# Performance work log

Hardware: AMD Instinct MI355X
Metric: run time of the kernel (lower is better)

The kernel has to match this reference:

```python
import jax, jax.numpy as jnp
import numpy as np

N_NODES = 20000
NUM_DRUGS = 2048
NUM_DPI = 200000
IN_C = 256
EMB = 256
HID = 512
OUT = 1
N_CL = 8
B = 16384


def setup_inputs() -> dict:
    key = jax.random.key(0)
    ks = jax.random.split(key, 10)
    x = jax.random.normal(ks[0], (N_NODES, IN_C), jnp.float32)
    # bipartite DPI edges: drug ids in [0, NUM_DRUGS), protein ids in [NUM_DRUGS, N_NODES)
    d = jax.random.randint(ks[1], (NUM_DPI,), 0, NUM_DRUGS)
    p = jax.random.randint(ks[2], (NUM_DPI,), NUM_DRUGS, N_NODES)
    edge_index = jnp.concatenate([jnp.stack([d, p]), jnp.stack([p, d])], axis=1)  # [2, 2*NUM_DPI]
    drug_drug_batch = jax.random.randint(ks[3], (2, B), 0, NUM_DRUGS)
    edge_cell_lines = jax.random.randint(ks[4], (B,), 0, N_CL)
    Wg1 = jax.random.normal(ks[5], (IN_C, EMB), jnp.float32) / np.float32(np.sqrt(IN_C))
    bg1 = jnp.zeros((EMB,), jnp.float32)
    Wg2 = jax.random.normal(ks[6], (EMB, EMB), jnp.float32) / np.float32(np.sqrt(EMB))
    bg2 = jnp.zeros((EMB,), jnp.float32)
    W1 = jax.random.normal(ks[7], (N_CL, 2 * EMB, HID), jnp.float32) / np.float32(np.sqrt(2 * EMB))
    b1 = jnp.zeros((N_CL, HID), jnp.float32)
    W2 = jax.random.normal(ks[8], (N_CL, HID, OUT), jnp.float32) / np.float32(np.sqrt(HID))
    b2 = jnp.zeros((N_CL, OUT), jnp.float32)
    return dict(x=x, edge_index=edge_index, drug_drug_batch=drug_drug_batch,
                edge_cell_lines=edge_cell_lines, num_drugs=NUM_DRUGS,
                Wg1=Wg1, bg1=bg1, Wg2=Wg2, bg2=bg2, W1=W1, b1=b1, W2=W2, b2=b2)


def _gcn(h_in, row, col, W, b, n):
    # PyG GCNConv: self-loops already appended to (row, col); symmetric normalization.
    h = h_in @ W  # [N, EMB]
    deg = jax.ops.segment_sum(jnp.ones(col.shape[0], h.dtype), col, num_segments=n)
    dinv = jnp.where(deg > 0, jax.lax.rsqrt(jnp.maximum(deg, 1e-12)), 0.0)
    msg = h[row] * (dinv[row] * dinv[col])[:, None]
    return jax.ops.segment_sum(msg, col, num_segments=n) + b


def reference(x, edge_index, drug_drug_batch, edge_cell_lines, num_drugs,
              Wg1, bg1, Wg2, bg2, W1, b1, W2, b2):
    n = x.shape[0]
    ar = jnp.arange(n, dtype=edge_index.dtype)
    row = jnp.concatenate([edge_index[0], ar])
    col = jnp.concatenate([edge_index[1], ar])
    h = jax.nn.relu(_gcn(x, row, col, Wg1, bg1, n))
    h = jax.nn.relu(_gcn(h, row, col, Wg2, bg2, n))
    # scatter-mean pool node embeddings of proteins into per-drug graph embeddings
    num_dpi = edge_index.shape[1] // 2
    avg = jnp.sort(edge_index[:, :num_dpi], axis=0)  # row0=drug id, row1=protein id
    node_emb = h[avg[1]]  # [NUM_DPI, EMB]
    sums = jax.ops.segment_sum(node_emb, avg[0], num_segments=num_drugs)
    cnt = jax.ops.segment_sum(jnp.ones(num_dpi, h.dtype), avg[0], num_segments=num_drugs)
    graph = sums / jnp.maximum(cnt, 1.0)[:, None]  # [NUM_DRUGS, EMB]
    xcat = jnp.concatenate([graph[drug_drug_batch[0]], graph[drug_drug_batch[1]]], axis=1)  # [B, 2*EMB]
    # per-cell-line MLP routing: run each expert over all rows, then gather per-row expert output
    n_cl = W1.shape[0]
    outs = jnp.stack([jax.nn.relu(xcat @ W1[c] + b1[c]) @ W2[c] + b2[c] for c in range(n_cl)])  # [C, B, OUT]
    preds = outs[edge_cell_lines, jnp.arange(xcat.shape[0])]  # [B, OUT]
    return preds
```

## Files before the change

### kernel.cpp

```cpp
#include <hip/hip_runtime.h>
#include <hip/hip_bf16.h>

#define N_NODES 20000
#define NUM_DRUGS 2048
#define N_PROT (N_NODES - NUM_DRUGS)
#define NUM_DPI 200000
#define E2 400000
#define CDIM 256
#define HID 512
#define N_CL 8
#define BATCH 16384
#define HN 8192

#define STRD 32
#define STRP 16
#define ELLD 192
#define ELLP 48

#define NB_T64 512
#define NB_TWG 32
#define NB_ZERO 79
#define NB_SPLIT 20000

typedef __attribute__((ext_vector_type(8))) short short8;
typedef __attribute__((ext_vector_type(4))) float floatx4;

__device__ inline unsigned short f2bf(float f) {
    unsigned u = __float_as_uint(f);
    u += 0x7fff + ((u >> 16) & 1);
    return (unsigned short)(u >> 16);
}
__device__ inline float bf2f(unsigned short h) {
    return __uint_as_float((unsigned)h << 16);
}
__device__ inline void split2(float v, unsigned short& h, unsigned short& l) {
    h = f2bf(v);
    l = f2bf(v - bf2f(h));
}
__device__ inline void gload16(const void* g, void* l) {
    __builtin_amdgcn_global_load_lds(
        (const __attribute__((address_space(1))) void*)g,
        (__attribute__((address_space(3))) void*)l, 16, 0, 0);
}
__device__ inline float4 f4fma(float4 v, float s, float4 a) {
    a.x = fmaf(v.x, s, a.x); a.y = fmaf(v.y, s, a.y);
    a.z = fmaf(v.z, s, a.z); a.w = fmaf(v.w, s, a.w);
    return a;
}
__device__ inline float4 bf4(const unsigned short* p) {
    ushort4 q = *(const ushort4*)p;
    return make_float4(bf2f(q.x), bf2f(q.y), bf2f(q.z), bf2f(q.w));
}

__global__ __launch_bounds__(256) void prep_all(
        const float* __restrict__ x, unsigned short* __restrict__ xhi,
        unsigned short* __restrict__ xlo,
        const float* __restrict__ Wg1, const float* __restrict__ Wg2,
        unsigned short* __restrict__ wg1Th, unsigned short* __restrict__ wg1Tl,
        unsigned short* __restrict__ wg2Th, unsigned short* __restrict__ wg2Tl,
        const float* __restrict__ W1, unsigned short* __restrict__ W1Th,
        unsigned short* __restrict__ W1Tl,
        int* __restrict__ cur_d, int* __restrict__ cur_p) {
    __shared__ float ld[64 * 65];
    int b = blockIdx.x;
    int t = threadIdx.x;
    int tx = t & 63, ty = t >> 6;
    if (b < NB_T64) {
        int m = b >> 5;
        int k0 = (b & 3) * 64, n0 = ((b >> 2) & 7) * 64;
        const float* Wm = W1 + (size_t)m * CDIM * HID;
#pragma unroll
        for (int rr = 0; rr < 16; rr++) {
            int kl = rr * 4 + ty;
            ld[tx * 65 + kl] = Wm[(size_t)(k0 + kl) * HID + n0 + tx];
        }
        __syncthreads();
        size_t obase = (size_t)m * HID * CDIM;
#pragma unroll
        for (int rr = 0; rr < 16; rr++) {
            int nl = rr * 4 + ty;
            float v = ld[nl * 65 + tx];
            unsigned short h, l;
            split2(v, h, l);
            size_t o = obase + (size_t)(n0 + nl) * CDIM + k0 + tx;
            W1Th[o] = h;
            W1Tl[o] = l;
        }
        return;
    }
    b -= NB_T64;
    if (b < NB_TWG) {
        const float* W = (b >> 4) ? Wg2 : Wg1;
        unsigned short* hi = (b >> 4) ? wg2Th : wg1Th;
        unsigned short* lo = (b >> 4) ? wg2Tl : wg1Tl;
        int k0 = (b & 3) * 64, n0 = ((b >> 2) & 3) * 64;
#pragma unroll
        for (int rr = 0; rr < 16; rr++) {
            int kl = rr * 4 + ty;
            ld[tx * 65 + kl] = W[(size_t)(k0 + kl) * CDIM + n0 + tx];
        }
        __syncthreads();
#pragma unroll
        for (int rr = 0; rr < 16; rr++) {
            int nl = rr * 4 + ty;
            float v = ld[nl * 65 + tx];
            unsigned short h, l;
            split2(v, h, l);
            size_t o = (size_t)(n0 + nl) * CDIM + k0 + tx;
            hi[o] = h;
            lo[o] = l;
        }
        return;
    }
    b -= NB_TWG;
    if (b < NB_ZERO) {
        int i = b * 256 + t;
        if (i < N_NODES) cur_p[i * STRP] = 0;
        if (i < NUM_DRUGS) cur_d[i * STRD] = 0;
        return;
    }
    b -= NB_ZERO;
    {
        int i = b * 256 + t;
        unsigned short h, l;
        split2(x[i], h, l);
        xhi[i] = h;
        xlo[i] = l;
    }
}

__global__ void fill_ell(const int* __restrict__ ei, int* cur_d, int* adj_drug,
                         int* cur_p, int* adj_prot) {
    int e = blockIdx.x * blockDim.x + threadIdx.x;
    if (e >= NUM_DPI) return;
    int d = ei[e];
    int p = ei[E2 + e];
    int posd = atomicAdd(&cur_d[d * STRD], 1);
    int posp = atomicAdd(&cur_p[p * STRP], 1);
    if (posd < ELLD) adj_drug[d * ELLD + posd] = p;
    if (posp < ELLP) adj_prot[(size_t)p * ELLP + posp] = d;
}

__global__ __launch_bounds__(256) void gemm_mfma(
        const unsigned short* __restrict__ Ahi, const unsigned short* __restrict__ Alo,
        const unsigned short* __restrict__ BThi, const unsigned short* __restrict__ BTlo,
        float* __restrict__ C, unsigned short* __restrict__ Cbf,
        int M, int K, int N, int mTiles,
        const int* __restrict__ cur_d, const int* __restrict__ cur_p,
        float* __restrict__ dinv) {
    if ((int)blockIdx.x >= mTiles) {
        int i = (((int)blockIdx.x - mTiles) * (int)gridDim.y + (int)blockIdx.y) * 256
                + (int)threadIdx.x;
        if (i < N_NODES) {
            int deg = (i < NUM_DRUGS) ? cur_d[i * STRD] : cur_p[i * STRP];
            dinv[i] = rsqrtf((float)(deg + 1));
        }
        return;
    }
    __shared__ unsigned short sAh[4096], sAl[4096], sBh[4096], sBl[4096];
    int t = threadIdx.x;
    int wv = t >> 6, lane = t & 63, quad = lane >> 4, l15 = lane & 15;
    int m0 = blockIdx.x * 128, n0 = blockIdx.y * 128;
    int m0w = (wv >> 1) * 64, n0w = (wv & 1) * 64;
    floatx4 zero = {0.f, 0.f, 0.f, 0.f};
    floatx4 acc[4][4];
#pragma unroll
    for (int i = 0; i < 4; i++)
#pragma unroll
        for (int j = 0; j < 4; j++) acc[i][j] = zero;

    for (int kk = 0; kk < K; kk += 32) {
#pragma unroll
        for (int c = 0; c < 2; c++) {
            int s = t + c * 256;
            int row = s >> 2, pos = s & 3;
            int ch = pos ^ ((row >> 1) & 3);
            int arow = m0 + row; if (arow > M - 1) arow = M - 1;
            int brow = n0 + row; if (brow > N - 1) brow = N - 1;
            size_t aoff = (size_t)arow * K + kk + ch * 8;
            size_t boff = (size_t)brow * K + kk + ch * 8;
            gload16(Ahi + aoff, &sAh[s * 8]);
            gload16(Alo + aoff, &sAl[s * 8]);
            gload16(BThi + boff, &sBh[s * 8]);
            gload16(BTlo + boff, &sBl[s * 8]);
        }
        __syncthreads();
        short8 ah[4], al[4], bh[4], bl[4];
        int posq = quad ^ ((l15 >> 1) & 3);
#pragma unroll
        for (int i = 0; i < 4; i++) {
            int sl = (m0w + i * 16 + l15) * 4 + posq;
            ah[i] = *(const short8*)&sAh[sl * 8];
            al[i] = *(const short8*)&sAl[sl * 8];
        }
#pragma unroll
        for (int j = 0; j < 4; j++) {
            int sl = (n0w + j * 16 + l15) * 4 + posq;
            bh[j] = *(const short8*)&sBh[sl * 8];
            bl[j] = *(const short8*)&sBl[sl * 8];
        }
#pragma unroll
        for (int i = 0; i < 4; i++)
#pragma unroll
            for (int j = 0; j < 4; j++) {
                acc[i][j] = __builtin_amdgcn_mfma_f32_16x16x32_bf16(ah[i], bh[j], acc[i][j], 0, 0, 0);
                acc[i][j] = __builtin_amdgcn_mfma_f32_16x16x32_bf16(ah[i], bl[j], acc[i][j], 0, 0, 0);
                acc[i][j] = __builtin_amdgcn_mfma_f32_16x16x32_bf16(al[i], bh[j], acc[i][j], 0, 0, 0);
            }
        __syncthreads();
    }
#pragma unroll
    for (int i = 0; i < 4; i++) {
        int gr = m0 + m0w + i * 16 + quad * 4;
#pragma unroll
        for (int r = 0; r < 4; r++) {
            if (gr + r < M) {
#pragma unroll
                for (int j = 0; j < 4; j++) {
                    size_t o = (size_t)(gr + r) * N + n0 + n0w + j * 16 + l15;
                    float v = acc[i][j][r];
                    if (C) C[o] = v;
                    if (Cbf) Cbf[o] = f2bf(v);
                }
            }
        }
    }
}

__global__ __launch_bounds__(256) void aggregate1(const float* __restrict__ tmp,
                                                  const unsigned short* __restrict__ tmpbf,
                                                  const int* __restrict__ cur_d,
                                                  const int* __restrict__ adj_drug,
                                                  const int* __restrict__ cur_p,
                                                  const int* __restrict__ adj_prot,
                                                  const float* __restrict__ dinv,
                                                  const float* __restrict__ bias,
                                                  unsigned short* __restrict__ outhi,
                                                  unsigned short* __restrict__ outlo) {
    int i = (blockIdx.x * blockDim.x + threadIdx.x) >> 6;
    int lane = threadIdx.x & 63;
    if (i >= N_NODES) return;
    float di = dinv[i];
    float4 a0 = make_float4(0.f, 0.f, 0.f, 0.f);
    float4 a1 = a0, a2 = a0, a3 = a0;
    if (i < NUM_DRUGS) {
        const int* adj = adj_drug + (size_t)i * ELLD;
        int e = cur_d[i * STRD];
        int idx = 0;
        for (; idx + 4 <= e; idx += 4) {
            int j0 = adj[idx + 0], j1 = adj[idx + 1];
            int j2 = adj[idx + 2], j3 = adj[idx + 3];
            float d0 = dinv[j0], d1 = dinv[j1], d2 = dinv[j2], d3 = dinv[j3];
            float4 v0 = bf4(&tmpbf[(size_t)j0 * CDIM + lane * 4]);
            float4 v1 = bf4(&tmpbf[(size_t)j1 * CDIM + lane * 4]);
            float4 v2 = bf4(&tmpbf[(size_t)j2 * CDIM + lane * 4]);
            float4 v3 = bf4(&tmpbf[(size_t)j3 * CDIM + lane * 4]);
            a0 = f4fma(v0, d0, a0);
            a1 = f4fma(v1, d1, a1);
            a2 = f4fma(v2, d2, a2);
            a3 = f4fma(v3, d3, a3);
        }
        for (; idx < e; idx++) {
            int j = adj[idx];
            a0 = f4fma(bf4(&tmpbf[(size_t)j * CDIM + lane * 4]), dinv[j], a0);
        }
    } else {
        const int* adj = adj_prot + (size_t)i * ELLP;
        int e = cur_p[i * STRP];
        int idx = 0;
        for (; idx + 4 <= e; idx += 4) {
            int j0 = adj[idx + 0], j1 = adj[idx + 1];
            int j2 = adj[idx + 2], j3 = adj[idx + 3];
            float d0 = dinv[j0], d1 = dinv[j1], d2 = dinv[j2], d3 = dinv[j3];
            float4 v0 = ((const float4*)(tmp + (size_t)j0 * CDIM))[lane];
            float4 v1 = ((const float4*)(tmp + (size_t)j1 * CDIM))[lane];
            float4 v2 = ((const float4*)(tmp + (size_t)j2 * CDIM))[lane];
            float4 v3 = ((const float4*)(tmp + (size_t)j3 * CDIM))[lane];
            a0 = f4fma(v0, d0, a0);
            a1 = f4fma(v1, d1, a1);
            a2 = f4fma(v2, d2, a2);
            a3 = f4fma(v3, d3, a3);
        }
        for (; idx < e; idx++) {
            int j = adj[idx];
            a0 = f4fma(((const float4*)(tmp + (size_t)j * CDIM))[lane], dinv[j], a0);
        }
    }
    float4 self = ((const float4*)(tmp + (size_t)i * CDIM))[lane];
    float4 acc;
    acc.x = (a0.x + a1.x) + (a2.x + a3.x) + self.x * di;
    acc.y = (a0.y + a1.y) + (a2.y + a3.y) + self.y * di;
    acc.z = (a0.z + a1.z) + (a2.z + a3.z) + self.z * di;
    acc.w = (a0.w + a1.w) + (a2.w + a3.w) + self.w * di;
    float4 bv = ((const float4*)bias)[lane];
    float4 r;
    r.x = fmaxf(fmaf(acc.x, di, bv.x), 0.f);
    r.y = fmaxf(fmaf(acc.y, di, bv.y), 0.f);
    r.z = fmaxf(fmaf(acc.z, di, bv.z), 0.f);
    r.w = fmaxf(fmaf(acc.w, di, bv.w), 0.f);
    ushort4 h, l;
    split2(r.x, h.x, l.x); split2(r.y, h.y, l.y);
    split2(r.z, h.z, l.z); split2(r.w, h.w, l.w);
    *(ushort4*)&outhi[(size_t)i * CDIM + lane * 4] = h;
    *(ushort4*)&outlo[(size_t)i * CDIM + lane * 4] = l;
}

__global__ __launch_bounds__(256) void aggregate2p(const float* __restrict__ tmp2,
                                                   const int* __restrict__ cur_p,
                                                   const int* __restrict__ adj_prot,
                                                   const float* __restrict__ dinv,
                                                   const float* __restrict__ bias,
                                                   unsigned short* __restrict__ h2bf) {
    int w = (blockIdx.x * blockDim.x + threadIdx.x) >> 6;
    int lane = threadIdx.x & 63;
    if (w >= N_PROT) return;
    int i = NUM_DRUGS + w;
    float di = dinv[i];
    float4 a0 = make_float4(0.f, 0.f, 0.f, 0.f);
    float4 a1 = a0, a2 = a0, a3 = a0;
    const int* adj = adj_prot + (size_t)i * ELLP;
    int e = cur_p[i * STRP];
    int idx = 0;
    for (; idx + 4 <= e; idx += 4) {
        int j0 = adj[idx + 0], j1 = adj[idx + 1];
        int j2 = adj[idx + 2], j3 = adj[idx + 3];
        float d0 = dinv[j0], d1 = dinv[j1], d2 = dinv[j2], d3 = dinv[j3];
        float4 v0 = ((const float4*)(tmp2 + (size_t)j0 * CDIM))[lane];
        float4 v1 = ((const float4*)(tmp2 + (size_t)j1 * CDIM))[lane];
        float4 v2 = ((const float4*)(tmp2 + (size_t)j2 * CDIM))[lane];
        float4 v3 = ((const float4*)(tmp2 + (size_t)j3 * CDIM))[lane];
        a0 = f4fma(v0, d0, a0);
        a1 = f4fma(v1, d1, a1);
        a2 = f4fma(v2, d2, a2);
        a3 = f4fma(v3, d3, a3);
    }
    for (; idx < e; idx++) {
        int j = adj[idx];
        a0 = f4fma(((const float4*)(tmp2 + (size_t)j * CDIM))[lane], dinv[j], a0);
    }
    float4 self = ((const float4*)(tmp2 + (size_t)i * CDIM))[lane];
    float4 acc;
    acc.x = (a0.x + a1.x) + (a2.x + a3.x) + self.x * di;
    acc.y = (a0.y + a1.y) + (a2.y + a3.y) + self.y * di;
    acc.z = (a0.z + a1.z) + (a2.z + a3.z) + self.z * di;
    acc.w = (a0.w + a1.w) + (a2.w + a3.w) + self.w * di;
    float4 bv = ((const float4*)bias)[lane];
    ushort4 o;
    o.x = f2bf(fmaxf(fmaf(acc.x, di, bv.x), 0.f));
    o.y = f2bf(fmaxf(fmaf(acc.y, di, bv.y), 0.f));
    o.z = f2bf(fmaxf(fmaf(acc.z, di, bv.z), 0.f));
    o.w = f2bf(fmaxf(fmaf(acc.w, di, bv.w), 0.f));
    *(ushort4*)&h2bf[(size_t)i * CDIM + lane * 4] = o;
}

__global__ __launch_bounds__(256) void pool_drugs(const unsigned short* __restrict__ h2bf,
                                                  unsigned short* __restrict__ Ghi,
                                                  unsigned short* __restrict__ Glo,
                                                  const int* __restrict__ cur_d,
                                                  const int* __restrict__ adj_drug) {
    __shared__ float4 red[4][64];
    int d = blockIdx.x;
    int w = threadIdx.x >> 6, lane = threadIdx.x & 63;
    const int* adj = adj_drug + (size_t)d * ELLD;
    int ecnt = cur_d[d * STRD];
    int e = ecnt < ELLD ? ecnt : ELLD;
    float4 a0 = make_float4(0.f, 0.f, 0.f, 0.f);
    float4 a1 = a0, a2 = a0, a3 = a0;
    int idx = w;
    for (; idx + 12 < e; idx += 16) {
        int j0 = adj[idx], j1 = adj[idx + 4], j2 = adj[idx + 8], j3 = adj[idx + 12];
        float4 v0 = bf4(&h2bf[(size_t)j0 * CDIM + lane * 4]);
        float4 v1 = bf4(&h2bf[(size_t)j1 * CDIM + lane * 4]);
        float4 v2 = bf4(&h2bf[(size_t)j2 * CDIM + lane * 4]);
        float4 v3 = bf4(&h2bf[(size_t)j3 * CDIM + lane * 4]);
        a0.x += v0.x; a0.y += v0.y; a0.z += v0.z; a0.w += v0.w;
        a1.x += v1.x; a1.y += v1.y; a1.z += v1.z; a1.w += v1.w;
        a2.x += v2.x; a2.y += v2.y; a2.z += v2.z; a2.w += v2.w;
        a3.x += v3.x; a3.y += v3.y; a3.z += v3.z; a3.w += v3.w;
    }
    for (; idx < e; idx += 4) {
        float4 v = bf4(&h2bf[(size_t)adj[idx] * CDIM + lane * 4]);
        a0.x += v.x; a0.y += v.y; a0.z += v.z; a0.w += v.w;
    }
    a0.x = (a0.x + a1.x) + (a2.x + a3.x);
    a0.y = (a0.y + a1.y) + (a2.y + a3.y);
    a0.z = (a0.z + a1.z) + (a2.z + a3.z);
    a0.w = (a0.w + a1.w) + (a2.w + a3.w);
    red[w][lane] = a0;
    __syncthreads();
    if (w == 0) {
        float4 r0 = red[0][lane], r1 = red[1][lane], r2 = red[2][lane], r3 = red[3][lane];
        float4 acc;
        acc.x = (r0.x + r1.x) + (r2.x + r3.x);
        acc.y = (r0.y + r1.y) + (r2.y + r3.y);
        acc.z = (r0.z + r1.z) + (r2.z + r3.z);
        acc.w = (r0.w + r1.w) + (r2.w + r3.w);
        float sc = 1.f / (float)(ecnt > 1 ? ecnt : 1);
        acc.x *= sc; acc.y *= sc; acc.z *= sc; acc.w *= sc;
        ushort4 h, l;
        split2(acc.x, h.x, l.x); split2(acc.y, h.y, l.y);
        split2(acc.z, h.z, l.z); split2(acc.w, h.w, l.w);
        *(ushort4*)&Ghi[(size_t)d * CDIM + lane * 4] = h;
        *(ushort4*)&Glo[(size_t)d * CDIM + lane * 4] = l;
    }
}

__global__ __launch_bounds__(256) void mlp_out(const unsigned short* __restrict__ Hbf,
                                               const int* __restrict__ ddb,
                                               const int* __restrict__ ecl,
                                               const float* __restrict__ b1,
                                               const float* __restrict__ W2,
                                               const float* __restrict__ b2,
                                               float* __restrict__ outp) {
    int r = (blockIdx.x * blockDim.x + threadIdx.x) >> 6;
    int lane = threadIdx.x & 63;
    if (r >= BATCH) return;
    int c = ecl[r];
    int d0 = ddb[r], d1 = ddb[BATCH + r];
    int n = lane * 8;
    const unsigned short* h0 = Hbf + (size_t)d0 * HN + (size_t)(c * 2) * HID + n;
    const unsigned short* h1 = Hbf + (size_t)d1 * HN + (size_t)(c * 2 + 1) * HID + n;
    const float* b1e = b1 + (size_t)c * HID + n;
    const float* w2e = W2 + (size_t)c * HID + n;
    short8 a8 = *(const short8*)h0;
    short8 b8 = *(const short8*)h1;
    float4 bb0 = *(const float4*)(b1e);
    float4 bb1 = *(const float4*)(b1e + 4);
    float4 w0 = *(const float4*)(w2e);
    float4 w1 = *(const float4*)(w2e + 4);
    float s = 0.f;
    float h;
    h = bf2f((unsigned short)a8[0]) + bf2f((unsigned short)b8[0]) + bb0.x;
    s = fmaf(fmaxf(h, 0.f), w0.x, s);
    h = bf2f((unsigned short)a8[1]) + bf2f((unsigned short)b8[1]) + bb0.y;
    s = fmaf(fmaxf(h, 0.f), w0.y, s);
    h = bf2f((unsigned short)a8[2]) + bf2f((unsigned short)b8[2]) + bb0.z;
    s = fmaf(fmaxf(h, 0.f), w0.z, s);
    h = bf2f((unsigned short)a8[3]) + bf2f((unsigned short)b8[3]) + bb0.w;
    s = fmaf(fmaxf(h, 0.f), w0.w, s);
    h = bf2f((unsigned short)a8[4]) + bf2f((unsigned short)b8[4]) + bb1.x;
    s = fmaf(fmaxf(h, 0.f), w1.x, s);
    h = bf2f((unsigned short)a8[5]) + bf2f((unsigned short)b8[5]) + bb1.y;
    s = fmaf(fmaxf(h, 0.f), w1.y, s);
    h = bf2f((unsigned short)a8[6]) + bf2f((unsigned short)b8[6]) + bb1.z;
    s = fmaf(fmaxf(h, 0.f), w1.z, s);
    h = bf2f((unsigned short)a8[7]) + bf2f((unsigned short)b8[7]) + bb1.w;
    s = fmaf(fmaxf(h, 0.f), w1.w, s);
    s += __shfl_xor(s, 1);
    s += __shfl_xor(s, 2);
    s += __shfl_xor(s, 4);
    s += __shfl_xor(s, 8);
    s += __shfl_xor(s, 16);
    s += __shfl_xor(s, 32);
    if (lane == 0) outp[r] = s + b2[c];
}

extern "C" void kernel_launch(void* const* d_in, const int* in_sizes, int n_in,
                              void* d_out, int out_size, void* d_ws, size_t ws_size,
                              hipStream_t stream) {
    const float* x   = (const float*)d_in[0];
    const int* ei    = (const int*)d_in[1];
    const int* ddb   = (const int*)d_in[2];
    const int* ecl   = (const int*)d_in[3];
    const float* Wg1 = (const float*)d_in[5];
    const float* bg1 = (const float*)d_in[6];
    const float* Wg2 = (const float*)d_in[7];
    const float* bg2 = (const float*)d_in[8];
    const float* W1  = (const float*)d_in[9];
    const float* b1  = (const float*)d_in[10];
    const float* W2  = (const float*)d_in[11];
    const float* b2  = (const float*)d_in[12];
    float* outp = (float*)d_out;

    const size_t NC = (size_t)N_NODES * CDIM;
    const size_t HRES = (size_t)NUM_DRUGS * HN * sizeof(float);
    char* r0 = (char*)d_ws;
    unsigned short* Hbf   = (unsigned short*)d_ws;
    float* tmp            = (float*)r0;
    unsigned short* t1bf  = (unsigned short*)(r0 + 20480000);
    unsigned short* h2bf  = t1bf;
    unsigned short* h1hi  = (unsigned short*)(r0 + 30720000);
    unsigned short* h1lo  = (unsigned short*)(r0 + 40960000);
    unsigned short* xhi   = h1hi;
    unsigned short* xlo   = h1lo;
    char* p = r0 + 51200000;
    auto alloc = [&](size_t bytes) {
        char* r = p;
        p += (bytes + 255) & ~size_t(255);
        return (void*)r;
    };
    float* dinv    = (float*)alloc(sizeof(float) * N_NODES);
    int* cur_d     = (int*)alloc(sizeof(int) * NUM_DRUGS * STRD);
    int* cur_p     = (int*)alloc(sizeof(int) * N_NODES * STRP);
    int* adj_drug  = (int*)alloc(sizeof(int) * NUM_DRUGS * ELLD);
    int* adj_prot  = (int*)alloc(sizeof(int) * (size_t)N_NODES * ELLP);
    p = (char*)d_ws + ((HRES + 255) & ~size_t(255));
    unsigned short* Ghi   = (unsigned short*)alloc(2 * NUM_DRUGS * CDIM);
    unsigned short* Glo   = (unsigned short*)alloc(2 * NUM_DRUGS * CDIM);
    unsigned short* wg1Th = (unsigned short*)alloc(2 * CDIM * CDIM);
    unsigned short* wg1Tl = (unsigned short*)alloc(2 * CDIM * CDIM);
    unsigned short* wg2Th = (unsigned short*)alloc(2 * CDIM * CDIM);
    unsigned short* wg2Tl = (unsigned short*)alloc(2 * CDIM * CDIM);
    unsigned short* W1Th  = (unsigned short*)alloc(2 * (size_t)N_CL * HID * HID);
    unsigned short* W1Tl  = (unsigned short*)alloc(2 * (size_t)N_CL * HID * HID);

    prep_all<<<NB_T64 + NB_TWG + NB_ZERO + NB_SPLIT, 256, 0, stream>>>(
        x, xhi, xlo, Wg1, Wg2, wg1Th, wg1Tl, wg2Th, wg2Tl, W1, W1Th, W1Tl,
        cur_d, cur_p);
    fill_ell<<<(NUM_DPI + 255) / 256, 256, 0, stream>>>(ei, cur_d, adj_drug,
                                                        cur_p, adj_prot);
    gemm_mfma<<<dim3(157 + 40, 2), 256, 0, stream>>>(
        xhi, xlo, wg1Th, wg1Tl, tmp, t1bf, N_NODES, CDIM, CDIM,
        157, cur_d, cur_p, dinv);
    aggregate1<<<(N_NODES * 64 + 255) / 256, 256, 0, stream>>>(
        tmp, t1bf, cur_d, adj_drug, cur_p, adj_prot, dinv, bg1, h1hi, h1lo);
    gemm_mfma<<<dim3(157, 2), 256, 0, stream>>>(
        h1hi, h1lo, wg2Th, wg2Tl, tmp, nullptr, N_NODES, CDIM, CDIM,
        157, nullptr, nullptr, nullptr);
    aggregate2p<<<(N_PROT * 64 + 255) / 256, 256, 0, stream>>>(
        tmp, cur_p, adj_prot, dinv, bg2, h2bf);
    pool_drugs<<<NUM_DRUGS, 256, 0, stream>>>(h2bf, Ghi, Glo, cur_d, adj_drug);
    gemm_mfma<<<dim3(NUM_DRUGS / 128, HN / 128), 256, 0, stream>>>(
        Ghi, Glo, W1Th, W1Tl, nullptr, Hbf, NUM_DRUGS, CDIM, HN,
        NUM_DRUGS / 128, nullptr, nullptr, nullptr);
    mlp_out<<<(BATCH * 64) / 256, 256, 0, stream>>>(Hbf, ddb, ecl, b1, W2, b2, outp);
}
```

Before: 267.3 us.

## Double-buffer GEMM LDS tiles and split drug aggregation across four wavefronts

```diff
diff --git a/kernel.cpp b/kernel.cpp
--- a/kernel.cpp
+++ b/kernel.cpp
@@ -21,6 +21,9 @@
 #define NB_TWG 32
 #define NB_ZERO 79
 #define NB_SPLIT 20000
+
+#define NB_AGG_D NUM_DRUGS
+#define NB_AGG_P ((N_PROT + 3) / 4)
 
 typedef __attribute__((ext_vector_type(8))) short short8;
 typedef __attribute__((ext_vector_type(4))) float floatx4;
@@ -157,7 +160,7 @@
         }
         return;
     }
-    __shared__ unsigned short sAh[4096], sAl[4096], sBh[4096], sBl[4096];
+    __shared__ unsigned short sAh[2][4096], sAl[2][4096], sBh[2][4096], sBl[2][4096];
     int t = threadIdx.x;
     int wv = t >> 6, lane = t & 63, quad = lane >> 4, l15 = lane & 15;
     int m0 = blockIdx.x * 128, n0 = blockIdx.y * 128;
@@ -169,7 +172,7 @@
 #pragma unroll
         for (int j = 0; j < 4; j++) acc[i][j] = zero;
 
-    for (int kk = 0; kk < K; kk += 32) {
+    auto STAGE = [&](int buf, int kk) {
 #pragma unroll
         for (int c = 0; c < 2; c++) {
             int s = t + c * 256;
@@ -179,25 +182,33 @@
             int brow = n0 + row; if (brow > N - 1) brow = N - 1;
             size_t aoff = (size_t)arow * K + kk + ch * 8;
             size_t boff = (size_t)brow * K + kk + ch * 8;
-            gload16(Ahi + aoff, &sAh[s * 8]);
-            gload16(Alo + aoff, &sAl[s * 8]);
-            gload16(BThi + boff, &sBh[s * 8]);
-            gload16(BTlo + boff, &sBl[s * 8]);
-        }
-        __syncthreads();
+            gload16(Ahi + aoff, &sAh[buf][s * 8]);
+            gload16(Alo + aoff, &sAl[buf][s * 8]);
+            gload16(BThi + boff, &sBh[buf][s * 8]);
+            gload16(BTlo + boff, &sBl[buf][s * 8]);
+        }
+    };
+
+    int nk = K >> 5;
+    STAGE(0, 0);
+    asm volatile("s_waitcnt vmcnt(0)" ::: "memory");
+    __builtin_amdgcn_s_barrier();
+    int cur = 0;
+    for (int it = 0; it < nk; ++it) {
+        if (it + 1 < nk) STAGE(cur ^ 1, (it + 1) << 5);
         short8 ah[4], al[4], bh[4], bl[4];
         int posq = quad ^ ((l15 >> 1) & 3);
 #pragma unroll
         for (int i = 0; i < 4; i++) {
             int sl = (m0w + i * 16 + l15) * 4 + posq;
-            ah[i] = *(const short8*)&sAh[sl * 8];
-            al[i] = *(const short8*)&sAl[sl * 8];
+            ah[i] = *(const short8*)&sAh[cur][sl * 8];
+            al[i] = *(const short8*)&sAl[cur][sl * 8];
         }
 #pragma unroll
         for (int j = 0; j < 4; j++) {
             int sl = (n0w + j * 16 + l15) * 4 + posq;
-            bh[j] = *(const short8*)&sBh[sl * 8];
-            bl[j] = *(const short8*)&sBl[sl * 8];
+            bh[j] = *(const short8*)&sBh[cur][sl * 8];
+            bl[j] = *(const short8*)&sBl[cur][sl * 8];
         }
 #pragma unroll
         for (int i = 0; i < 4; i++)
@@ -207,7 +218,11 @@
                 acc[i][j] = __builtin_amdgcn_mfma_f32_16x16x32_bf16(ah[i], bl[j], acc[i][j], 0, 0, 0);
                 acc[i][j] = __builtin_amdgcn_mfma_f32_16x16x32_bf16(al[i], bh[j], acc[i][j], 0, 0, 0);
             }
-        __syncthreads();
+        if (it + 1 < nk) {
+            asm volatile("s_waitcnt vmcnt(0)" ::: "memory");
+            __builtin_amdgcn_s_barrier();
+            cur ^= 1;
+        }
     }
 #pragma unroll
     for (int i = 0; i < 4; i++) {
@@ -237,19 +252,20 @@
                                                   const float* __restrict__ bias,
                                                   unsigned short* __restrict__ outhi,
                                                   unsigned short* __restrict__ outlo) {
-    int i = (blockIdx.x * blockDim.x + threadIdx.x) >> 6;
+    __shared__ float4 red[4][64];
+    int b = blockIdx.x;
     int lane = threadIdx.x & 63;
-    if (i >= N_NODES) return;
-    float di = dinv[i];
-    float4 a0 = make_float4(0.f, 0.f, 0.f, 0.f);
-    float4 a1 = a0, a2 = a0, a3 = a0;
-    if (i < NUM_DRUGS) {
-        const int* adj = adj_drug + (size_t)i * ELLD;
-        int e = cur_d[i * STRD];
-        int idx = 0;
-        for (; idx + 4 <= e; idx += 4) {
-            int j0 = adj[idx + 0], j1 = adj[idx + 1];
-            int j2 = adj[idx + 2], j3 = adj[idx + 3];
+    if (b < NB_AGG_D) {
+        int d = b;
+        int w = threadIdx.x >> 6;
+        const int* adj = adj_drug + (size_t)d * ELLD;
+        int ecnt = cur_d[d * STRD];
+        int e = ecnt < ELLD ? ecnt : ELLD;
+        float4 a0 = make_float4(0.f, 0.f, 0.f, 0.f);
+        float4 a1 = a0, a2 = a0, a3 = a0;
+        int idx = w;
+        for (; idx + 12 < e; idx += 16) {
+            int j0 = adj[idx], j1 = adj[idx + 4], j2 = adj[idx + 8], j3 = adj[idx + 12];
             float d0 = dinv[j0], d1 = dinv[j1], d2 = dinv[j2], d3 = dinv[j3];
             float4 v0 = bf4(&tmpbf[(size_t)j0 * CDIM + lane * 4]);
             float4 v1 = bf4(&tmpbf[(size_t)j1 * CDIM + lane * 4]);
@@ -260,31 +276,63 @@
             a2 = f4fma(v2, d2, a2);
             a3 = f4fma(v3, d3, a3);
         }
-        for (; idx < e; idx++) {
+        for (; idx < e; idx += 4) {
             int j = adj[idx];
             a0 = f4fma(bf4(&tmpbf[(size_t)j * CDIM + lane * 4]), dinv[j], a0);
         }
-    } else {
-        const int* adj = adj_prot + (size_t)i * ELLP;
-        int e = cur_p[i * STRP];
-        int idx = 0;
-        for (; idx + 4 <= e; idx += 4) {
-            int j0 = adj[idx + 0], j1 = adj[idx + 1];
-            int j2 = adj[idx + 2], j3 = adj[idx + 3];
-            float d0 = dinv[j0], d1 = dinv[j1], d2 = dinv[j2], d3 = dinv[j3];
-            float4 v0 = ((const float4*)(tmp + (size_t)j0 * CDIM))[lane];
-            float4 v1 = ((const float4*)(tmp + (size_t)j1 * CDIM))[lane];
-            float4 v2 = ((const float4*)(tmp + (size_t)j2 * CDIM))[lane];
-            float4 v3 = ((const float4*)(tmp + (size_t)j3 * CDIM))[lane];
-            a0 = f4fma(v0, d0, a0);
-            a1 = f4fma(v1, d1, a1);
-            a2 = f4fma(v2, d2, a2);
-            a3 = f4fma(v3, d3, a3);
-        }
-        for (; idx < e; idx++) {
-            int j = adj[idx];
-            a0 = f4fma(((const float4*)(tmp + (size_t)j * CDIM))[lane], dinv[j], a0);
-        }
+        a0.x = (a0.x + a1.x) + (a2.x + a3.x);
+        a0.y = (a0.y + a1.y) + (a2.y + a3.y);
+        a0.z = (a0.z + a1.z) + (a2.z + a3.z);
+        a0.w = (a0.w + a1.w) + (a2.w + a3.w);
+        red[w][lane] = a0;
+        __syncthreads();
+        if (w == 0) {
+            float di = dinv[d];
+            float4 r0 = red[0][lane], r1 = red[1][lane], r2 = red[2][lane], r3 = red[3][lane];
+            float4 self = ((const float4*)(tmp + (size_t)d * CDIM))[lane];
+            float4 acc;
+            acc.x = (r0.x + r1.x) + (r2.x + r3.x) + self.x * di;
+            acc.y = (r0.y + r1.y) + (r2.y + r3.y) + self.y * di;
+            acc.z = (r0.z + r1.z) + (r2.z + r3.z) + self.z * di;
+            acc.w = (r0.w + r1.w) + (r2.w + r3.w) + self.w * di;
+            float4 bv = ((const float4*)bias)[lane];
+            float4 r;
+            r.x = fmaxf(fmaf(acc.x, di, bv.x), 0.f);
+            r.y = fmaxf(fmaf(acc.y, di, bv.y), 0.f);
+            r.z = fmaxf(fmaf(acc.z, di, bv.z), 0.f);
+            r.w = fmaxf(fmaf(acc.w, di, bv.w), 0.f);
+            ushort4 h, l;
+            split2(r.x, h.x, l.x); split2(r.y, h.y, l.y);
+            split2(r.z, h.z, l.z); split2(r.w, h.w, l.w);
+            *(ushort4*)&outhi[(size_t)d * CDIM + lane * 4] = h;
+            *(ushort4*)&outlo[(size_t)d * CDIM + lane * 4] = l;
+        }
+        return;
+    }
+    int i = NUM_DRUGS + (b - NB_AGG_D) * 4 + (threadIdx.x >> 6);
+    if (i >= N_NODES) return;
+    float di = dinv[i];
+    float4 a0 = make_float4(0.f, 0.f, 0.f, 0.f);
+    float4 a1 = a0, a2 = a0, a3 = a0;
+    const int* adj = adj_prot + (size_t)i * ELLP;
+    int e = cur_p[i * STRP];
+    int idx = 0;
+    for (; idx + 4 <= e; idx += 4) {
+        int j0 = adj[idx + 0], j1 = adj[idx + 1];
+        int j2 = adj[idx + 2], j3 = adj[idx + 3];
+        float d0 = dinv[j0], d1 = dinv[j1], d2 = dinv[j2], d3 = dinv[j3];
+        float4 v0 = ((const float4*)(tmp + (size_t)j0 * CDIM))[lane];
+        float4 v1 = ((const float4*)(tmp + (size_t)j1 * CDIM))[lane];
+        float4 v2 = ((const float4*)(tmp + (size_t)j2 * CDIM))[lane];
+        float4 v3 = ((const float4*)(tmp + (size_t)j3 * CDIM))[lane];
+        a0 = f4fma(v0, d0, a0);
+        a1 = f4fma(v1, d1, a1);
+        a2 = f4fma(v2, d2, a2);
+        a3 = f4fma(v3, d3, a3);
+    }
+    for (; idx < e; idx++) {
+        int j = adj[idx];
+        a0 = f4fma(((const float4*)(tmp + (size_t)j * CDIM))[lane], dinv[j], a0);
     }
     float4 self = ((const float4*)(tmp + (size_t)i * CDIM))[lane];
     float4 acc;
@@ -512,7 +560,7 @@
     gemm_mfma<<<dim3(157 + 40, 2), 256, 0, stream>>>(
         xhi, xlo, wg1Th, wg1Tl, tmp, t1bf, N_NODES, CDIM, CDIM,
         157, cur_d, cur_p, dinv);
-    aggregate1<<<(N_NODES * 64 + 255) / 256, 256, 0, stream>>>(
+    aggregate1<<<NB_AGG_D + NB_AGG_P, 256, 0, stream>>>(
         tmp, t1bf, cur_d, adj_drug, cur_p, adj_prot, dinv, bg1, h1hi, h1lo);
     gemm_mfma<<<dim3(157, 2), 256, 0, stream>>>(
         h1hi, h1lo, wg2Th, wg2Tl, tmp, nullptr, N_NODES, CDIM, CDIM,
```

Result: faster. 257.7 us (-3.6%).
